# Kernel tuning notes

Hardware: AMD Instinct MI355X
Metric: run time of the kernel (lower is better)

The kernel has to match this reference:

```python
import jax, jax.numpy as jnp
import numpy as np

EPS = 1e-5


def _layernorm(x, w, b):
    mu = jnp.mean(x, axis=-1, keepdims=True)
    xc = x - mu
    var = jnp.mean(xc * xc, axis=-1, keepdims=True)
    return xc * jax.lax.rsqrt(var + EPS) * w + b


def _s5_ssm(u, lam_re, lam_im, log_step, B_re, B_im, C_re, C_im, Dvec):
    # u: [B,L,D]; diagonal complex SSM with ZOH discretization + associative scan
    Lam = lam_re + 1j * lam_im                      # [P]
    step = jnp.exp(log_step)                        # [P]
    Abar = jnp.exp(Lam * step)                      # [P]
    Bbar = ((Abar - 1.0) / Lam)[:, None] * (B_re + 1j * B_im)  # [P,D]
    Bu = jnp.einsum('bld,pd->blp', u.astype(jnp.complex64), Bbar)  # [B,L,P]
    A_el = jnp.broadcast_to(Abar, Bu.shape)

    def binop(e1, e2):
        a1, b1 = e1
        a2, b2 = e2
        return a1 * a2, a2 * b1 + b2

    _, xs = jax.lax.associative_scan(binop, (A_el, Bu), axis=1)  # [B,L,P] complex
    y = jnp.einsum('blp,dp->bld', xs, C_re + 1j * C_im).real + Dvec * u
    return y


def _s5_block(x, an_w, an_b, lam_re, lam_im, log_step, B_re, B_im, C_re, C_im,
              Dvec, fn_w, fn_b, Wenc, Wdec):
    fx = _layernorm(x, an_w, an_b)
    s = _s5_ssm(fx, lam_re, lam_im, log_step, B_re, B_im, C_re, C_im, Dvec)
    z = jax.nn.gelu(s, approximate=False) + fx
    fy = _layernorm(z, fn_w, fn_b)
    h = fy @ Wenc.T                                  # [B,L,2D]
    a, g = jnp.split(h, 2, axis=-1)                  # GEGLU
    return (a * jax.nn.gelu(g, approximate=False)) @ Wdec.T + fy


def setup_inputs() -> dict:
    D = 1048   # d_model
    P = 1048   # state_dim
    NL = 3
    Bsz, L = 4, 4096
    key = jax.random.key(0)
    ks = jax.random.split(key, 20)
    f32 = jnp.float32
    inp = {}
    inp['x'] = jax.random.normal(ks[0], (Bsz, L, 1), f32)
    inp['enc_w'] = jax.random.normal(ks[1], (D, 1), f32)
    inp['enc_b'] = jnp.zeros((D,), f32)
    inp['norm_w'] = jnp.ones((NL, D), f32)
    inp['norm_b'] = jnp.zeros((NL, D), f32)
    inp['attn_norm_w'] = jnp.ones((NL, D), f32)
    inp['attn_norm_b'] = jnp.zeros((NL, D), f32)
    inp['ff_norm_w'] = jnp.ones((NL, D), f32)
    inp['ff_norm_b'] = jnp.zeros((NL, D), f32)
    # stable diagonal dynamics: Re(Lambda) < 0
    inp['lam_re'] = -0.5 * jax.random.uniform(ks[2], (NL, P), f32) - 0.05
    inp['lam_im'] = np.float32(np.pi) * jax.random.normal(ks[3], (NL, P), f32)
    lo, hi = np.float32(np.log(1e-3)), np.float32(np.log(1e-1))
    inp['log_step'] = lo + (hi - lo) * jax.random.uniform(ks[4], (NL, P), f32)
    sB = np.float32(1.0 / np.sqrt(D))
    sC = np.float32(1.0 / np.sqrt(P))
    inp['B_re'] = sB * jax.random.normal(ks[5], (NL, P, D), f32)
    inp['B_im'] = sB * jax.random.normal(ks[6], (NL, P, D), f32)
    inp['C_re'] = sC * jax.random.normal(ks[7], (NL, D, P), f32)
    inp['C_im'] = sC * jax.random.normal(ks[8], (NL, D, P), f32)
    inp['Dvec'] = jax.random.normal(ks[9], (NL, D), f32)
    sW = np.float32(1.0 / np.sqrt(D))
    inp['Wenc'] = sW * jax.random.normal(ks[10], (NL, 2 * D, D), f32)
    inp['Wdec'] = sW * jax.random.normal(ks[11], (NL, D, D), f32)
    inp['head_w'] = sW * jax.random.normal(ks[12], (1, D), f32)
    inp['head_b'] = jnp.zeros((1,), f32)
    return inp


def reference(x, enc_w, enc_b, norm_w, norm_b, attn_norm_w, attn_norm_b,
              ff_norm_w, ff_norm_b, lam_re, lam_im, log_step, B_re, B_im,
              C_re, C_im, Dvec, Wenc, Wdec, head_w, head_b):
    h = x @ enc_w.T + enc_b                          # [B,L,D]
    n_layers = norm_w.shape[0]
    for i in range(n_layers):                        # small fixed loop over layers
        z = _layernorm(h, norm_w[i], norm_b[i])      # prenorm
        z = _s5_block(z, attn_norm_w[i], attn_norm_b[i], lam_re[i], lam_im[i],
                      log_step[i], B_re[i], B_im[i], C_re[i], C_im[i],
                      Dvec[i], ff_norm_w[i], ff_norm_b[i], Wenc[i], Wdec[i])
        h = h + z                                    # residual (dropout = identity in eval)
    pooled = jnp.mean(h, axis=1)                     # [B,D]
    y = (pooled @ head_w.T + head_b).squeeze(-1)     # [B]
    return y
```

## Files before the change

### kernel.cpp

```cpp
#include <hip/hip_runtime.h>
#include <hip/hip_bf16.h>
#include <cstddef>

typedef __hip_bfloat16 bf16;

#define D_MODEL 1048
#define P_DIM   1048
#define NLAYER  3
#define BSZ     4
#define LSEQ    4096
#define BL      (BSZ*LSEQ)
#define BLD     ((size_t)BL*D_MODEL)
#define KP      1056
#define NP      1152
#define BLA     ((size_t)BL*KP)
#define NPKP    ((size_t)NP*KP)

#define NC      64
#define CL      (LSEQ/NC)
#define NSCAN   (BSZ*NC*P_DIM)
#define P2      (P_DIM/2)
#define NSCAN2  (BSZ*NC*P2)

typedef __attribute__((ext_vector_type(8))) short short8;
typedef __attribute__((ext_vector_type(4))) float f32x4;

#define TM 128
#define TN 128
#define TK 32
#define TILE_SH (TM*TK)
#define NGEMM   ((BL/TM)*(NP/TN))
#define KSTEPS  (KP/TK)

__device__ __forceinline__ float gelu_f(float x) {
    return 0.5f * x * (1.f + erff(x * 0.70710678118654752f));
}

__device__ __forceinline__ void tile_coords(int id, int& m0, int& n0) {
    int xcd  = id & 7;
    int slot = id >> 3;
    int xg   = slot / 9;
    int j    = slot - xg*9;
    m0 = (xg*8 + xcd) * TM;
    n0 = j * TN;
}

__device__ __forceinline__ void stage_tile(
    const bf16* __restrict__ src, int row0, int k0, short* lds, int tid)
{
#pragma unroll
    for (int c = 0; c < 2; ++c) {
        int chunk = tid + 256*c;
        int r = chunk >> 2;
        int col = ((chunk ^ (r >> 1)) & 3) * 8;
        __builtin_amdgcn_global_load_lds(
            (const __attribute__((address_space(1))) void*)(src + (size_t)(row0 + r)*KP + k0 + col),
            (__attribute__((address_space(3))) void*)(lds + chunk*8), 16, 0, 0);
    }
}

__device__ __forceinline__ void stage512(
    const bf16* __restrict__ src, int row0, int k0, short* lds, int tid)
{
    int r = tid >> 2;
    int col = ((tid ^ (r >> 1)) & 3) * 8;
    __builtin_amdgcn_global_load_lds(
        (const __attribute__((address_space(1))) void*)(src + (size_t)(row0 + r)*KP + k0 + col),
        (__attribute__((address_space(3))) void*)(lds + tid*8), 16, 0, 0);
}

__device__ __forceinline__ void mfma_step1(
    const short* As, const short* Ws, f32x4 (&acc)[4][4],
    int wm, int wn, int row_in, int qs)
{
    short8 a[4], b[4];
#pragma unroll
    for (int i = 0; i < 4; ++i) {
        a[i] = *(const short8*)&As[(wm + i*16 + row_in)*TK + qs];
        b[i] = *(const short8*)&Ws[(wn + i*16 + row_in)*TK + qs];
    }
#pragma unroll
    for (int i = 0; i < 4; ++i)
#pragma unroll
        for (int j = 0; j < 4; ++j)
            acc[i][j] = __builtin_amdgcn_mfma_f32_16x16x32_bf16(a[i], b[j], acc[i][j], 0, 0, 0);
}

#define ROT3(p0, p1, p2) { short* _t = p0; p0 = p1; p1 = p2; p2 = _t; }

template <int MODE>
__global__ __launch_bounds__(512, 4) void gemm2o_k(
    const bf16* __restrict__ A, const bf16* __restrict__ W0,
    const bf16* __restrict__ W1,
    bf16* __restrict__ O0, bf16* __restrict__ O1, int N)
{
    __shared__ __align__(16) short smem[9*TILE_SH];
    short *pA  = smem,             *pA1  = smem + TILE_SH,   *pA2  = smem + 2*TILE_SH;
    short *pW0 = smem + 3*TILE_SH, *pW01 = smem + 4*TILE_SH, *pW02 = smem + 5*TILE_SH;
    short *pW1 = smem + 6*TILE_SH, *pW11 = smem + 7*TILE_SH, *pW12 = smem + 8*TILE_SH;
    const int tid  = threadIdx.x;
    int m0, n0;
    tile_coords(blockIdx.x, m0, n0);
    const int wave = tid >> 6, lane = tid & 63;
    const int wr = wave >> 2, wc = wave & 3;
    const int wm = wr * 64;
    const int wn = (wc & 1) * 64;
    const bool useW1 = (wc >= 2);
    const int row_in = lane & 15;
    const int qs = (((lane >> 4) ^ (lane >> 1)) & 3) * 8;

    f32x4 acc[4][4] = {};

    stage512(A,  m0, 0,    pA,   tid);
    stage512(W0, n0, 0,    pW0,  tid);
    stage512(W1, n0, 0,    pW1,  tid);
    stage512(A,  m0, TK,   pA1,  tid);
    stage512(W0, n0, TK,   pW01, tid);
    stage512(W1, n0, TK,   pW11, tid);
    stage512(A,  m0, 2*TK, pA2,  tid);
    stage512(W0, n0, 2*TK, pW02, tid);
    stage512(W1, n0, 2*TK, pW12, tid);

    for (int s = 0; s <= KSTEPS - 4; ++s) {
        asm volatile("s_waitcnt vmcnt(6)" ::: "memory");
        __builtin_amdgcn_s_barrier();
        mfma_step1(pA, useW1 ? pW1 : pW0, acc, wm, wn, row_in, qs);
        __builtin_amdgcn_s_barrier();
        const int k0 = (s + 3) * TK;
        stage512(A,  m0, k0, pA,  tid);
        stage512(W0, n0, k0, pW0, tid);
        stage512(W1, n0, k0, pW1, tid);
        ROT3(pA,  pA1,  pA2);
        ROT3(pW0, pW01, pW02);
        ROT3(pW1, pW11, pW12);
    }
    asm volatile("s_waitcnt vmcnt(6)" ::: "memory");
    __builtin_amdgcn_s_barrier();
    mfma_step1(pA, useW1 ? pW1 : pW0, acc, wm, wn, row_in, qs);
    asm volatile("s_waitcnt vmcnt(3)" ::: "memory");
    __builtin_amdgcn_s_barrier();
    mfma_step1(pA1, useW1 ? pW11 : pW01, acc, wm, wn, row_in, qs);
    asm volatile("s_waitcnt vmcnt(0)" ::: "memory");
    __builtin_amdgcn_s_barrier();
    mfma_step1(pA2, useW1 ? pW12 : pW02, acc, wm, wn, row_in, qs);

    const int quad = lane >> 4;
    if (MODE == 0) {
        bf16* O = useW1 ? O1 : O0;
#pragma unroll
        for (int i = 0; i < 4; ++i) {
#pragma unroll
            for (int j = 0; j < 4; ++j) {
                int n = n0 + wn + j*16 + row_in;
#pragma unroll
                for (int r = 0; r < 4; ++r) {
                    int m = m0 + wm + i*16 + quad*4 + r;
                    size_t o = (size_t)m*KP + n;
                    if (n < N)        O[o] = __float2bfloat16(acc[i][j][r]);
                    else if (n < KP)  O[o] = __float2bfloat16(0.f);
                }
            }
        }
    } else {
        f32x4* xb = (f32x4*)smem;
        const int pp = wr*2 + (wc & 1);
#pragma unroll
        for (int ih = 0; ih < 2; ++ih) {
            __syncthreads();
            if (useW1) {
#pragma unroll
                for (int il = 0; il < 2; ++il)
#pragma unroll
                    for (int j = 0; j < 4; ++j)
                        xb[(((pp*2 + il)*4 + j) << 6) + lane] = acc[2*ih + il][j];
            }
            __syncthreads();
            if (!useW1) {
#pragma unroll
                for (int il = 0; il < 2; ++il) {
                    int i = 2*ih + il;
#pragma unroll
                    for (int j = 0; j < 4; ++j) {
                        f32x4 g = xb[(((pp*2 + il)*4 + j) << 6) + lane];
                        int n = n0 + wn + j*16 + row_in;
#pragma unroll
                        for (int r = 0; r < 4; ++r) {
                            int m = m0 + wm + i*16 + quad*4 + r;
                            size_t o = (size_t)m*KP + n;
                            if (n < N)        O0[o] = __float2bfloat16(acc[i][j][r] * gelu_f(g[r]));
                            else if (n < KP)  O0[o] = __float2bfloat16(0.f);
                        }
                    }
                }
            }
        }
    }
}

__global__ __launch_bounds__(256, 2) void gemmC_k(
    const bf16* __restrict__ A0, const bf16* __restrict__ W0,
    const bf16* __restrict__ A1, const bf16* __restrict__ W1,
    const bf16* __restrict__ fx, const float* __restrict__ dv,
    bf16* __restrict__ O, int N)
{
    __shared__ __align__(16) short As[2][TILE_SH];
    __shared__ __align__(16) short Ws[2][TILE_SH];
    const int tid  = threadIdx.x;
    int m0, n0;
    tile_coords(blockIdx.x, m0, n0);
    const int wave = tid >> 6, lane = tid & 63;
    const int wm = (wave >> 1) * 64, wn = (wave & 1) * 64;
    const int row_in = lane & 15;
    const int qs = (((lane >> 4) ^ (lane >> 1)) & 3) * 8;

    f32x4 acc[4][4] = {};

    const int NST = 2*KSTEPS;
    stage_tile(A0, m0, 0,  As[0], tid);
    stage_tile(W0, n0, 0,  Ws[0], tid);
    stage_tile(A0, m0, TK, As[1], tid);
    stage_tile(W0, n0, TK, Ws[1], tid);

    for (int s = 0; s < NST - 1; ++s) {
        asm volatile("s_waitcnt vmcnt(4)" ::: "memory");
        __builtin_amdgcn_s_barrier();
        mfma_step1(As[s & 1], Ws[s & 1], acc, wm, wn, row_in, qs);
        __builtin_amdgcn_s_barrier();
        if (s < NST - 2) {
            int t = s + 2;
            const bf16* A = (t >= KSTEPS) ? A1 : A0;
            const bf16* W = (t >= KSTEPS) ? W1 : W0;
            int kk = (t >= KSTEPS) ? t - KSTEPS : t;
            stage_tile(A, m0, kk*TK, As[s & 1], tid);
            stage_tile(W, n0, kk*TK, Ws[s & 1], tid);
        }
    }
    asm volatile("s_waitcnt vmcnt(0)" ::: "memory");
    __builtin_amdgcn_s_barrier();
    mfma_step1(As[(NST-1) & 1], Ws[(NST-1) & 1], acc, wm, wn, row_in, qs);

    const int quad = lane >> 4;
#pragma unroll
    for (int i = 0; i < 4; ++i) {
#pragma unroll
        for (int j = 0; j < 4; ++j) {
            int n = n0 + wn + j*16 + row_in;
#pragma unroll
            for (int r = 0; r < 4; ++r) {
                int m = m0 + wm + i*16 + quad*4 + r;
                size_t o = (size_t)m*KP + n;
                if (n < N) {
                    float f = __bfloat162float(fx[o]);
                    float t = acc[i][j][r] + dv[n]*f;
                    O[o] = __float2bfloat16(gelu_f(t) + f);
                } else if (n < KP) {
                    O[o] = __float2bfloat16(0.f);
                }
            }
        }
    }
}

__global__ __launch_bounds__(256, 2) void gemmD_k(
    const bf16* __restrict__ A, const bf16* __restrict__ W,
    const bf16* __restrict__ fy, float* __restrict__ h, int N)
{
    __shared__ __align__(16) short As[2][TILE_SH];
    __shared__ __align__(16) short Ws[2][TILE_SH];
    const int tid  = threadIdx.x;
    int m0, n0;
    tile_coords(blockIdx.x, m0, n0);
    const int wave = tid >> 6, lane = tid & 63;
    const int wm = (wave >> 1) * 64, wn = (wave & 1) * 64;
    const int row_in = lane & 15;
    const int qs = (((lane >> 4) ^ (lane >> 1)) & 3) * 8;

    f32x4 acc[4][4] = {};

    stage_tile(A, m0, 0,  As[0], tid);
    stage_tile(W, n0, 0,  Ws[0], tid);
    stage_tile(A, m0, TK, As[1], tid);
    stage_tile(W, n0, TK, Ws[1], tid);

    for (int s = 0; s < KSTEPS - 1; ++s) {
        asm volatile("s_waitcnt vmcnt(4)" ::: "memory");
        __builtin_amdgcn_s_barrier();
        mfma_step1(As[s & 1], Ws[s & 1], acc, wm, wn, row_in, qs);
        __builtin_amdgcn_s_barrier();
        if (s < KSTEPS - 2) {
            const int k0 = (s + 2) * TK;
            stage_tile(A, m0, k0, As[s & 1], tid);
            stage_tile(W, n0, k0, Ws[s & 1], tid);
        }
    }
    asm volatile("s_waitcnt vmcnt(0)" ::: "memory");
    __builtin_amdgcn_s_barrier();
    mfma_step1(As[(KSTEPS-1) & 1], Ws[(KSTEPS-1) & 1], acc, wm, wn, row_in, qs);

    const int quad = lane >> 4;
#pragma unroll
    for (int i = 0; i < 4; ++i) {
#pragma unroll
        for (int j = 0; j < 4; ++j) {
            int n = n0 + wn + j*16 + row_in;
            if (n >= N) continue;
#pragma unroll
            for (int r = 0; r < 4; ++r) {
                int m = m0 + wm + i*16 + quad*4 + r;
                float f = __bfloat162float(fy[(size_t)m*KP + n]);
                h[(size_t)m*D_MODEL + n] += acc[i][j][r] + f;
            }
        }
    }
}

__global__ __launch_bounds__(256) void prepconv_k(
    const float* __restrict__ lam_re, const float* __restrict__ lam_im,
    const float* __restrict__ log_step,
    const float* __restrict__ B_re, const float* __restrict__ B_im,
    bf16* __restrict__ bbar_re, bf16* __restrict__ bbar_im,
    float* __restrict__ abar,
    const float* __restrict__ s0, const float* __restrict__ s1,
    const float* __restrict__ s2, const float* __restrict__ s3,
    const float* __restrict__ s4, bf16* __restrict__ w5)
{
    size_t idx = (size_t)blockIdx.x*256 + threadIdx.x;
    if (idx >= NPKP) return;
    int z = blockIdx.z;
    int p = (int)(idx / KP);
    int d = (int)(idx - (size_t)p*KP);
    if (z == 0) {
        if (p >= P_DIM || d >= D_MODEL) {
            bbar_re[idx] = __float2bfloat16(0.f);
            bbar_im[idx] = __float2bfloat16(0.f);
            return;
        }
        float lr = lam_re[p], li = lam_im[p];
        float st = expf(log_step[p]);
        float er = expf(lr*st);
        float ar = er * cosf(li*st);
        float ai = er * sinf(li*st);
        if (d == 0) { abar[p] = ar; abar[P_DIM + p] = ai; }
        float den = lr*lr + li*li;
        float xr = ar - 1.f, xi = ai;
        float cr = (xr*lr + xi*li) / den;
        float ci = (xi*lr - xr*li) / den;
        float br = B_re[(size_t)p*D_MODEL + d], bi = B_im[(size_t)p*D_MODEL + d];
        bbar_re[idx] = __float2bfloat16(cr*br - ci*bi);
        bbar_im[idx] = __float2bfloat16(cr*bi + ci*br);
    } else {
        int w = z - 1;
        const float* src = (w == 0) ? s0 : (w == 1) ? s1 : (w == 2) ? s2 : (w == 3) ? s3 : s4;
        float scale = (w == 1) ? -1.f : 1.f;
        float v = (p < D_MODEL && d < D_MODEL) ? scale*src[(size_t)p*D_MODEL + d] : 0.f;
        w5[(size_t)w*NPKP + idx] = __float2bfloat16(v);
    }
}

__device__ __forceinline__ float2 block_reduce2(float a, float b) {
    __syncthreads();
    for (int off = 32; off; off >>= 1) {
        a += __shfl_down(a, off, 64);
        b += __shfl_down(b, off, 64);
    }
    __shared__ float sa[4], sb[4];
    int lane = threadIdx.x & 63, wv = threadIdx.x >> 6;
    if (lane == 0) { sa[wv] = a; sb[wv] = b; }
    __syncthreads();
    if (threadIdx.x == 0) {
        sa[0] = sa[0]+sa[1]+sa[2]+sa[3];
        sb[0] = sb[0]+sb[1]+sb[2]+sb[3];
    }
    __syncthreads();
    return make_float2(sa[0], sb[0]);
}

template <int ENC>
__global__ __launch_bounds__(256) void ln2x_k(
    const float* __restrict__ xin,
    const float* __restrict__ ew, const float* __restrict__ eb,
    float* __restrict__ hbuf,
    const float* __restrict__ w1, const float* __restrict__ bb1,
    const float* __restrict__ w2, const float* __restrict__ bb2,
    bf16* __restrict__ y)
{
    const size_t row = blockIdx.x;
    float v[5];
    float s = 0.f, ss = 0.f;
    int i = 0;
    if (ENC) {
        float xv = xin[row];
        float* hr = hbuf + row * D_MODEL;
        for (int d = threadIdx.x; d < KP; d += 256, ++i) {
            float t = 0.f;
            if (d < D_MODEL) { t = xv*ew[d] + eb[d]; hr[d] = t; }
            v[i] = t; s += t; ss += t*t;
        }
    } else {
        const float* xr = hbuf + row * D_MODEL;
        for (int d = threadIdx.x; d < KP; d += 256, ++i) {
            float t = (d < D_MODEL) ? xr[d] : 0.f;
            v[i] = t; s += t; ss += t*t;
        }
    }
    float2 r = block_reduce2(s, ss);
    float mu  = r.x * (1.f/D_MODEL);
    float var = r.y * (1.f/D_MODEL) - mu*mu;
    float inv = rsqrtf(var + 1e-5f);
    s = 0.f; ss = 0.f; i = 0;
    for (int d = threadIdx.x; d < KP; d += 256, ++i) {
        float z = (d < D_MODEL) ? (v[i]-mu)*inv*w1[d] + bb1[d] : 0.f;
        v[i] = z; s += z; ss += z*z;
    }
    r = block_reduce2(s, ss);
    mu  = r.x * (1.f/D_MODEL);
    var = r.y * (1.f/D_MODEL) - mu*mu;
    inv = rsqrtf(var + 1e-5f);
    bf16* yr = y + row * KP;
    i = 0;
    for (int d = threadIdx.x; d < KP; d += 256, ++i) {
        float o = (d < D_MODEL) ? (v[i]-mu)*inv*w2[d] + bb2[d] : 0.f;
        yr[d] = __float2bfloat16(o);
    }
}

__global__ __launch_bounds__(256) void ln_k(
    const bf16* __restrict__ x, const float* __restrict__ w,
    const float* __restrict__ b, bf16* __restrict__ y)
{
    const size_t row = blockIdx.x;
    const bf16* xr = x + row * KP;
    float v[5];
    float s = 0.f, ss = 0.f;
    int i = 0;
    for (int d = threadIdx.x; d < KP; d += 256, ++i) {
        float t = (d < D_MODEL) ? __bfloat162float(xr[d]) : 0.f;
        v[i] = t; s += t; ss += t*t;
    }
    float2 r = block_reduce2(s, ss);
    float mu  = r.x * (1.f/D_MODEL);
    float var = r.y * (1.f/D_MODEL) - mu*mu;
    float inv = rsqrtf(var + 1e-5f);
    bf16* yr = y + row * KP;
    i = 0;
    for (int d = threadIdx.x; d < KP; d += 256, ++i) {
        float o = (d < D_MODEL) ? (v[i]-mu)*inv*w[d] + b[d] : 0.f;
        yr[d] = __float2bfloat16(o);
    }
}

__device__ __forceinline__ float2 bf2f(unsigned int u) {
    unsigned int lo = u << 16, hi = u & 0xffff0000u;
    float2 r;
    r.x = __uint_as_float(lo);
    r.y = __uint_as_float(hi);
    return r;
}
__device__ __forceinline__ unsigned int f2bf2(float a, float b) {
    bf16 ba = __float2bfloat16(a), bb = __float2bfloat16(b);
    unsigned short ua = *(unsigned short*)&ba, ub = *(unsigned short*)&bb;
    return (unsigned int)ua | ((unsigned int)ub << 16);
}

__global__ __launch_bounds__(256) void scan_partial_k(
    const unsigned int* __restrict__ ur, const unsigned int* __restrict__ ui,
    const float* __restrict__ abar,
    float* __restrict__ sum_re, float* __restrict__ sum_im)
{
    int idx = blockIdx.x*256 + threadIdx.x;
    if (idx >= NSCAN2) return;
    int p2 = idx % P2;
    int rest = idx / P2;
    int c = rest % NC, b = rest / NC;
    int p = 2*p2;
    float ar0 = abar[p],   ai0 = abar[P_DIM + p];
    float ar1 = abar[p+1], ai1 = abar[P_DIM + p + 1];
    size_t base = (((size_t)b*LSEQ + (size_t)c*CL)*KP + p) >> 1;
    float s0r = 0.f, s0i = 0.f, s1r = 0.f, s1i = 0.f;
    for (int i = 0; i < CL; ++i) {
        size_t o = base + (size_t)i*(KP/2);
        float2 br = bf2f(ur[o]);
        float2 bi = bf2f(ui[o]);
        float n0r = fmaf(ar0, s0r, fmaf(-ai0, s0i, br.x));
        float n0i = fmaf(ar0, s0i, fmaf( ai0, s0r, bi.x));
        float n1r = fmaf(ar1, s1r, fmaf(-ai1, s1i, br.y));
        float n1i = fmaf(ar1, s1i, fmaf( ai1, s1r, bi.y));
        s0r = n0r; s0i = n0i; s1r = n1r; s1i = n1i;
    }
    size_t so = ((size_t)b*NC + c)*P_DIM + p;
    *(float2*)&sum_re[so] = make_float2(s0r, s1r);
    *(float2*)&sum_im[so] = make_float2(s0i, s1i);
}

__global__ __launch_bounds__(256) void scan_carry_k(
    const float* __restrict__ sum_re, const float* __restrict__ sum_im,
    const float* __restrict__ abar,
    float* __restrict__ car_re, float* __restrict__ car_im)
{
    int idx = blockIdx.x*256 + threadIdx.x;
    if (idx >= BSZ*P_DIM) return;
    int p = idx % P_DIM, b = idx / P_DIM;
    float cr = abar[p], ci = abar[P_DIM + p];
#pragma unroll
    for (int s = 0; s < 6; ++s) {
        float nr = cr*cr - ci*ci;
        float ni = 2.f*cr*ci;
        cr = nr; ci = ni;
    }
    float xre = 0.f, xim = 0.f;
    size_t base = (size_t)b*NC*P_DIM + p;
    for (int c = 0; c < NC; ++c) {
        size_t o = base + (size_t)c*P_DIM;
        car_re[o] = xre; car_im[o] = xim;
        float sre = sum_re[o], sim = sum_im[o];
        float nr = fmaf(cr, xre, fmaf(-ci, xim, sre));
        float ni = fmaf(cr, xim, fmaf( ci, xre, sim));
        xre = nr; xim = ni;
    }
}

__global__ __launch_bounds__(256) void scan_apply_k(
    unsigned int* __restrict__ ur, unsigned int* __restrict__ ui,
    const float* __restrict__ abar,
    const float* __restrict__ car_re, const float* __restrict__ car_im)
{
    int idx = blockIdx.x*256 + threadIdx.x;
    if (idx >= NSCAN2) return;
    int p2 = idx % P2;
    int rest = idx / P2;
    int c = rest % NC, b = rest / NC;
    int p = 2*p2;
    float ar0 = abar[p],   ai0 = abar[P_DIM + p];
    float ar1 = abar[p+1], ai1 = abar[P_DIM + p + 1];
    size_t co = ((size_t)b*NC + c)*P_DIM + p;
    float2 c_r = *(const float2*)&car_re[co];
    float2 c_i = *(const float2*)&car_im[co];
    float x0r = c_r.x, x0i = c_i.x, x1r = c_r.y, x1i = c_i.y;
    size_t base = (((size_t)b*LSEQ + (size_t)c*CL)*KP + p) >> 1;
    for (int i = 0; i < CL; ++i) {
        size_t o = base + (size_t)i*(KP/2);
        float2 br = bf2f(ur[o]);
        float2 bi = bf2f(ui[o]);
        float n0r = fmaf(ar0, x0r, fmaf(-ai0, x0i, br.x));
        float n0i = fmaf(ar0, x0i, fmaf( ai0, x0r, bi.x));
        float n1r = fmaf(ar1, x1r, fmaf(-ai1, x1i, br.y));
        float n1i = fmaf(ar1, x1i, fmaf( ai1, x1r, bi.y));
        x0r = n0r; x0i = n0i; x1r = n1r; x1i = n1i;
        ur[o] = f2bf2(x0r, x1r);
        ui[o] = f2bf2(x0i, x1i);
    }
}

__global__ void head_init_k(float* out, const float* hb)
{
    if (threadIdx.x < BSZ) out[threadIdx.x] = hb[0];
}

__global__ __launch_bounds__(256) void head_k(
    const float* __restrict__ h, const float* __restrict__ hw,
    float* __restrict__ out)
{
    int b = blockIdx.x;
    int chunk = blockIdx.y;
    const float* hb = h + ((size_t)b*LSEQ + (size_t)chunk*64)*D_MODEL;
    float s = 0.f;
    for (int l = 0; l < 64; ++l) {
        const float* hr = hb + (size_t)l*D_MODEL;
        for (int d = threadIdx.x; d < D_MODEL; d += 256)
            s += hr[d]*hw[d];
    }
    for (int off = 32; off; off >>= 1) s += __shfl_down(s, off, 64);
    __shared__ float sm[4];
    int lane = threadIdx.x & 63, wv = threadIdx.x >> 6;
    if (lane == 0) sm[wv] = s;
    __syncthreads();
    if (threadIdx.x == 0)
        atomicAdd(out + b, (sm[0]+sm[1]+sm[2]+sm[3]) * (1.f/LSEQ));
}

extern "C" void kernel_launch(void* const* d_in, const int* in_sizes, int n_in,
                              void* d_out, int out_size, void* d_ws, size_t ws_size,
                              hipStream_t stream)
{
    const float* x          = (const float*)d_in[0];
    const float* enc_w      = (const float*)d_in[1];
    const float* enc_b      = (const float*)d_in[2];
    const float* norm_w     = (const float*)d_in[3];
    const float* norm_b     = (const float*)d_in[4];
    const float* attn_w     = (const float*)d_in[5];
    const float* attn_b     = (const float*)d_in[6];
    const float* ff_w       = (const float*)d_in[7];
    const float* ff_b       = (const float*)d_in[8];
    const float* lam_re     = (const float*)d_in[9];
    const float* lam_im     = (const float*)d_in[10];
    const float* log_step   = (const float*)d_in[11];
    const float* B_re       = (const float*)d_in[12];
    const float* B_im       = (const float*)d_in[13];
    const float* C_re       = (const float*)d_in[14];
    const float* C_im       = (const float*)d_in[15];
    const float* Dvec       = (const float*)d_in[16];
    const float* Wenc       = (const float*)d_in[17];
    const float* Wdec       = (const float*)d_in[18];
    const float* head_w     = (const float*)d_in[19];
    const float* head_b     = (const float*)d_in[20];
    float* out = (float*)d_out;

    float* h    = (float*)d_ws;
    bf16*  b1   = (bf16*)(h + BLD);
    bf16*  b2   = b1 + BLA;
    bf16*  b3   = b2 + BLA;
    bf16*  b4   = b3 + BLA;
    bf16*  wbr  = b4 + BLA;
    bf16*  wbi  = wbr + NPKP;
    bf16*  w5   = wbi + NPKP;
    bf16*  wcr  = w5;
    bf16*  wci  = w5 + NPKP;
    bf16*  wea  = w5 + 2*NPKP;
    bf16*  weg  = w5 + 3*NPKP;
    bf16*  wd   = w5 + 4*NPKP;
    float* abar = (float*)(w5 + 5*NPKP);
    float* sum_re = abar + 2*P_DIM;
    float* sum_im = sum_re + NSCAN;
    float* car_re = sum_im + NSCAN;
    float* car_im = car_re + NSCAN;

    const int CV   = (int)((NPKP + 255)/256);
    const int SC_G = (NSCAN2 + 255)/256;
    const size_t pd = (size_t)P_DIM*D_MODEL;

    for (int i = 0; i < NLAYER; ++i) {
        const float* WencA = Wenc + (size_t)i*2*pd;
        const float* WencG = WencA + pd;
        prepconv_k<<<dim3(CV,1,6), 256, 0, stream>>>(
            lam_re + i*P_DIM, lam_im + i*P_DIM, log_step + i*P_DIM,
            B_re + i*pd, B_im + i*pd, wbr, wbi, abar,
            C_re + i*pd, C_im + i*pd, WencA, WencG, Wdec + i*pd, w5);

        if (i == 0)
            ln2x_k<1><<<BL, 256, 0, stream>>>(x, enc_w, enc_b, h,
                norm_w + i*D_MODEL, norm_b + i*D_MODEL,
                attn_w + i*D_MODEL, attn_b + i*D_MODEL, b2);
        else
            ln2x_k<0><<<BL, 256, 0, stream>>>(nullptr, nullptr, nullptr, h,
                norm_w + i*D_MODEL, norm_b + i*D_MODEL,
                attn_w + i*D_MODEL, attn_b + i*D_MODEL, b2);

        gemm2o_k<0><<<NGEMM, 512, 0, stream>>>(b2, wbr, wbi, b1, b3, P_DIM);

        scan_partial_k<<<SC_G, 256, 0, stream>>>((unsigned int*)b1, (unsigned int*)b3,
                                                 abar, sum_re, sum_im);
        scan_carry_k<<<(BSZ*P_DIM + 255)/256, 256, 0, stream>>>(sum_re, sum_im, abar, car_re, car_im);
        scan_apply_k<<<SC_G, 256, 0, stream>>>((unsigned int*)b1, (unsigned int*)b3,
                                               abar, car_re, car_im);

        gemmC_k<<<NGEMM, 256, 0, stream>>>(b1, wcr, b3, wci, b2, Dvec + i*D_MODEL, b4, D_MODEL);

        ln_k<<<BL, 256, 0, stream>>>(b4, ff_w + i*D_MODEL, ff_b + i*D_MODEL, b1);

        gemm2o_k<1><<<NGEMM, 512, 0, stream>>>(b1, wea, weg, b2, nullptr, D_MODEL);

        gemmD_k<<<NGEMM, 256, 0, stream>>>(b2, wd, b1, h, D_MODEL);
    }

    head_init_k<<<1, 64, 0, stream>>>(out, head_b);
    head_k<<<dim3(BSZ, 64), 256, 0, stream>>>(h, head_w, out);
}
```

Measured before the change: 1.916 ms.

## Enlarge GEMM tiles to 256x128 with 128x64 per-wave subtiles and MFMA priority

Doubles the M tile of all three GEMM kernels to 256 rows, so each wave now computes a 128x64 subtile with 8x4 MFMA accumulators. This reuses each staged W fragment across more A rows and cuts global and LDS traffic per FLOP. The dual-output kernel drops its triple-buffered pipeline for double buffering, and s_setprio is raised around the MFMA blocks. In exchange, per-thread register pressure roughly doubles and occupancy falls (launch bounds go from 4 to 2 blocks for gemm2o). Halving the tile count also risks poorer CU load balance.

```diff
diff --git a/kernel.cpp b/kernel.cpp
--- a/kernel.cpp
+++ b/kernel.cpp
@@ -25,12 +25,15 @@
 typedef __attribute__((ext_vector_type(8))) short short8;
 typedef __attribute__((ext_vector_type(4))) float f32x4;
 
-#define TM 128
+#define TM 256
 #define TN 128
 #define TK 32
-#define TILE_SH (TM*TK)
-#define NGEMM   ((BL/TM)*(NP/TN))
+#define ASH2 (TM*TK)
+#define WSH  (TN*TK)
+#define SLOTC (ASH2 + WSH)
+#define SLOT2 (ASH2 + 2*WSH)
 #define KSTEPS  (KP/TK)
+#define NGEMM ((BL/TM)*(NP/TN))
 
 __device__ __forceinline__ float gelu_f(float x) {
     return 0.5f * x * (1.f + erff(x * 0.70710678118654752f));
@@ -45,21 +48,46 @@
     n0 = j * TN;
 }
 
-__device__ __forceinline__ void stage_tile(
+__device__ __forceinline__ void stageA_t256(
     const bf16* __restrict__ src, int row0, int k0, short* lds, int tid)
 {
 #pragma unroll
-    for (int c = 0; c < 2; ++c) {
-        int chunk = tid + 256*c;
-        int r = chunk >> 2;
-        int col = ((chunk ^ (r >> 1)) & 3) * 8;
+    for (int c0 = 0; c0 < 4; ++c0) {
+        int c = tid + 256*c0;
+        int r = c >> 2;
+        int col = ((c ^ (r >> 1)) & 3) * 8;
         __builtin_amdgcn_global_load_lds(
             (const __attribute__((address_space(1))) void*)(src + (size_t)(row0 + r)*KP + k0 + col),
-            (__attribute__((address_space(3))) void*)(lds + chunk*8), 16, 0, 0);
-    }
-}
-
-__device__ __forceinline__ void stage512(
+            (__attribute__((address_space(3))) void*)(lds + c*8), 16, 0, 0);
+    }
+}
+__device__ __forceinline__ void stageW_t256(
+    const bf16* __restrict__ src, int row0, int k0, short* lds, int tid)
+{
+#pragma unroll
+    for (int c0 = 0; c0 < 2; ++c0) {
+        int c = tid + 256*c0;
+        int r = c >> 2;
+        int col = ((c ^ (r >> 1)) & 3) * 8;
+        __builtin_amdgcn_global_load_lds(
+            (const __attribute__((address_space(1))) void*)(src + (size_t)(row0 + r)*KP + k0 + col),
+            (__attribute__((address_space(3))) void*)(lds + c*8), 16, 0, 0);
+    }
+}
+__device__ __forceinline__ void stageA_t512(
+    const bf16* __restrict__ src, int row0, int k0, short* lds, int tid)
+{
+#pragma unroll
+    for (int c0 = 0; c0 < 2; ++c0) {
+        int c = tid + 512*c0;
+        int r = c >> 2;
+        int col = ((c ^ (r >> 1)) & 3) * 8;
+        __builtin_amdgcn_global_load_lds(
+            (const __attribute__((address_space(1))) void*)(src + (size_t)(row0 + r)*KP + k0 + col),
+            (__attribute__((address_space(3))) void*)(lds + c*8), 16, 0, 0);
+    }
+}
+__device__ __forceinline__ void stageW_t512(
     const bf16* __restrict__ src, int row0, int k0, short* lds, int tid)
 {
     int r = tid >> 2;
@@ -69,86 +97,74 @@
         (__attribute__((address_space(3))) void*)(lds + tid*8), 16, 0, 0);
 }
 
-__device__ __forceinline__ void mfma_step1(
-    const short* As, const short* Ws, f32x4 (&acc)[4][4],
+__device__ __forceinline__ void mfma_big(
+    const short* As, const short* Ws, f32x4 (&acc)[8][4],
     int wm, int wn, int row_in, int qs)
 {
-    short8 a[4], b[4];
-#pragma unroll
-    for (int i = 0; i < 4; ++i) {
+    short8 a[8], b[4];
+#pragma unroll
+    for (int i = 0; i < 8; ++i)
         a[i] = *(const short8*)&As[(wm + i*16 + row_in)*TK + qs];
-        b[i] = *(const short8*)&Ws[(wn + i*16 + row_in)*TK + qs];
-    }
-#pragma unroll
-    for (int i = 0; i < 4; ++i)
+#pragma unroll
+    for (int j = 0; j < 4; ++j)
+        b[j] = *(const short8*)&Ws[(wn + j*16 + row_in)*TK + qs];
+#pragma unroll
+    for (int i = 0; i < 8; ++i)
 #pragma unroll
         for (int j = 0; j < 4; ++j)
             acc[i][j] = __builtin_amdgcn_mfma_f32_16x16x32_bf16(a[i], b[j], acc[i][j], 0, 0, 0);
 }
 
-#define ROT3(p0, p1, p2) { short* _t = p0; p0 = p1; p1 = p2; p2 = _t; }
-
 template <int MODE>
-__global__ __launch_bounds__(512, 4) void gemm2o_k(
+__global__ __launch_bounds__(512, 2) void gemm2o_k(
     const bf16* __restrict__ A, const bf16* __restrict__ W0,
     const bf16* __restrict__ W1,
     bf16* __restrict__ O0, bf16* __restrict__ O1, int N)
 {
-    __shared__ __align__(16) short smem[9*TILE_SH];
-    short *pA  = smem,             *pA1  = smem + TILE_SH,   *pA2  = smem + 2*TILE_SH;
-    short *pW0 = smem + 3*TILE_SH, *pW01 = smem + 4*TILE_SH, *pW02 = smem + 5*TILE_SH;
-    short *pW1 = smem + 6*TILE_SH, *pW11 = smem + 7*TILE_SH, *pW12 = smem + 8*TILE_SH;
+    __shared__ __align__(16) short smem[2*SLOT2];
     const int tid  = threadIdx.x;
     int m0, n0;
     tile_coords(blockIdx.x, m0, n0);
     const int wave = tid >> 6, lane = tid & 63;
-    const int wr = wave >> 2, wc = wave & 3;
-    const int wm = wr * 64;
-    const int wn = (wc & 1) * 64;
-    const bool useW1 = (wc >= 2);
+    const int g = wave >> 2;
+    const int u = wave & 3;
+    const int wm = (u >> 1) * 128, wn = (u & 1) * 64;
     const int row_in = lane & 15;
     const int qs = (((lane >> 4) ^ (lane >> 1)) & 3) * 8;
 
-    f32x4 acc[4][4] = {};
-
-    stage512(A,  m0, 0,    pA,   tid);
-    stage512(W0, n0, 0,    pW0,  tid);
-    stage512(W1, n0, 0,    pW1,  tid);
-    stage512(A,  m0, TK,   pA1,  tid);
-    stage512(W0, n0, TK,   pW01, tid);
-    stage512(W1, n0, TK,   pW11, tid);
-    stage512(A,  m0, 2*TK, pA2,  tid);
-    stage512(W0, n0, 2*TK, pW02, tid);
-    stage512(W1, n0, 2*TK, pW12, tid);
-
-    for (int s = 0; s <= KSTEPS - 4; ++s) {
-        asm volatile("s_waitcnt vmcnt(6)" ::: "memory");
+    f32x4 acc[8][4] = {};
+
+#define STG2(s) { int _s=(s); short* _b = smem + (_s&1)*SLOT2; \
+    stageA_t512(A,  m0, _s*TK, _b, tid); \
+    stageW_t512(W0, n0, _s*TK, _b + ASH2, tid); \
+    stageW_t512(W1, n0, _s*TK, _b + ASH2 + WSH, tid); }
+
+    STG2(0); STG2(1);
+    for (int s = 0; s < KSTEPS - 1; ++s) {
+        asm volatile("s_waitcnt vmcnt(4)" ::: "memory");
         __builtin_amdgcn_s_barrier();
-        mfma_step1(pA, useW1 ? pW1 : pW0, acc, wm, wn, row_in, qs);
+        short* base = smem + (s & 1)*SLOT2;
+        __builtin_amdgcn_s_setprio(1);
+        mfma_big(base, base + ASH2 + g*WSH, acc, wm, wn, row_in, qs);
+        __builtin_amdgcn_s_setprio(0);
         __builtin_amdgcn_s_barrier();
-        const int k0 = (s + 3) * TK;
-        stage512(A,  m0, k0, pA,  tid);
-        stage512(W0, n0, k0, pW0, tid);
-        stage512(W1, n0, k0, pW1, tid);
-        ROT3(pA,  pA1,  pA2);
-        ROT3(pW0, pW01, pW02);
-        ROT3(pW1, pW11, pW12);
-    }
-    asm volatile("s_waitcnt vmcnt(6)" ::: "memory");
-    __builtin_amdgcn_s_barrier();
-    mfma_step1(pA, useW1 ? pW1 : pW0, acc, wm, wn, row_in, qs);
-    asm volatile("s_waitcnt vmcnt(3)" ::: "memory");
-    __builtin_amdgcn_s_barrier();
-    mfma_step1(pA1, useW1 ? pW11 : pW01, acc, wm, wn, row_in, qs);
+        if (s < KSTEPS - 2) STG2(s + 2);
+    }
     asm volatile("s_waitcnt vmcnt(0)" ::: "memory");
     __builtin_amdgcn_s_barrier();
-    mfma_step1(pA2, useW1 ? pW12 : pW02, acc, wm, wn, row_in, qs);
+    {
+        short* base = smem + ((KSTEPS-1) & 1)*SLOT2;
+        __builtin_amdgcn_s_setprio(1);
+        mfma_big(base, base + ASH2 + g*WSH, acc, wm, wn, row_in, qs);
+        __builtin_amdgcn_s_setprio(0);
+    }
+#undef STG2
 
     const int quad = lane >> 4;
     if (MODE == 0) {
-        bf16* O = useW1 ? O1 : O0;
-#pragma unroll
-        for (int i = 0; i < 4; ++i) {
+        bf16* O = g ? O1 : O0;
+#pragma unroll
+        for (int i = 0; i < 8; ++i) {
 #pragma unroll
             for (int j = 0; j < 4; ++j) {
                 int n = n0 + wn + j*16 + row_in;
@@ -163,31 +179,30 @@
         }
     } else {
         f32x4* xb = (f32x4*)smem;
-        const int pp = wr*2 + (wc & 1);
-#pragma unroll
-        for (int ih = 0; ih < 2; ++ih) {
+#pragma unroll
+        for (int ih = 0; ih < 4; ++ih) {
             __syncthreads();
-            if (useW1) {
+            if (g) {
 #pragma unroll
                 for (int il = 0; il < 2; ++il)
 #pragma unroll
                     for (int j = 0; j < 4; ++j)
-                        xb[(((pp*2 + il)*4 + j) << 6) + lane] = acc[2*ih + il][j];
+                        xb[(((u*2 + il)*4 + j) << 6) + lane] = acc[2*ih + il][j];
             }
             __syncthreads();
-            if (!useW1) {
+            if (!g) {
 #pragma unroll
                 for (int il = 0; il < 2; ++il) {
                     int i = 2*ih + il;
 #pragma unroll
                     for (int j = 0; j < 4; ++j) {
-                        f32x4 g = xb[(((pp*2 + il)*4 + j) << 6) + lane];
+                        f32x4 gv = xb[(((u*2 + il)*4 + j) << 6) + lane];
                         int n = n0 + wn + j*16 + row_in;
 #pragma unroll
                         for (int r = 0; r < 4; ++r) {
                             int m = m0 + wm + i*16 + quad*4 + r;
                             size_t o = (size_t)m*KP + n;
-                            if (n < N)        O0[o] = __float2bfloat16(acc[i][j][r] * gelu_f(g[r]));
+                            if (n < N)        O0[o] = __float2bfloat16(acc[i][j][r] * gelu_f(gv[r]));
                             else if (n < KP)  O0[o] = __float2bfloat16(0.f);
                         }
                     }
@@ -203,45 +218,50 @@
     const bf16* __restrict__ fx, const float* __restrict__ dv,
     bf16* __restrict__ O, int N)
 {
-    __shared__ __align__(16) short As[2][TILE_SH];
-    __shared__ __align__(16) short Ws[2][TILE_SH];
+    __shared__ __align__(16) short smem[2*SLOTC];
     const int tid  = threadIdx.x;
     int m0, n0;
     tile_coords(blockIdx.x, m0, n0);
     const int wave = tid >> 6, lane = tid & 63;
-    const int wm = (wave >> 1) * 64, wn = (wave & 1) * 64;
+    const int wm = (wave >> 1) * 128, wn = (wave & 1) * 64;
     const int row_in = lane & 15;
     const int qs = (((lane >> 4) ^ (lane >> 1)) & 3) * 8;
 
-    f32x4 acc[4][4] = {};
+    f32x4 acc[8][4] = {};
 
     const int NST = 2*KSTEPS;
-    stage_tile(A0, m0, 0,  As[0], tid);
-    stage_tile(W0, n0, 0,  Ws[0], tid);
-    stage_tile(A0, m0, TK, As[1], tid);
-    stage_tile(W0, n0, TK, Ws[1], tid);
-
+#define STGC(s) { int _s=(s); \
+    const bf16* _A = (_s >= KSTEPS) ? A1 : A0; \
+    const bf16* _W = (_s >= KSTEPS) ? W1 : W0; \
+    int _kk = (_s >= KSTEPS ? _s - KSTEPS : _s)*TK; \
+    short* _b = smem + (_s&1)*SLOTC; \
+    stageA_t256(_A, m0, _kk, _b, tid); \
+    stageW_t256(_W, n0, _kk, _b + ASH2, tid); }
+
+    STGC(0); STGC(1);
     for (int s = 0; s < NST - 1; ++s) {
-        asm volatile("s_waitcnt vmcnt(4)" ::: "memory");
+        asm volatile("s_waitcnt vmcnt(6)" ::: "memory");
         __builtin_amdgcn_s_barrier();
-        mfma_step1(As[s & 1], Ws[s & 1], acc, wm, wn, row_in, qs);
+        short* base = smem + (s & 1)*SLOTC;
+        __builtin_amdgcn_s_setprio(1);
+        mfma_big(base, base + ASH2, acc, wm, wn, row_in, qs);
+        __builtin_amdgcn_s_setprio(0);
         __builtin_amdgcn_s_barrier();
-        if (s < NST - 2) {
-            int t = s + 2;
-            const bf16* A = (t >= KSTEPS) ? A1 : A0;
-            const bf16* W = (t >= KSTEPS) ? W1 : W0;
-            int kk = (t >= KSTEPS) ? t - KSTEPS : t;
-            stage_tile(A, m0, kk*TK, As[s & 1], tid);
-            stage_tile(W, n0, kk*TK, Ws[s & 1], tid);
-        }
+        if (s < NST - 2) STGC(s + 2);
     }
     asm volatile("s_waitcnt vmcnt(0)" ::: "memory");
     __builtin_amdgcn_s_barrier();
-    mfma_step1(As[(NST-1) & 1], Ws[(NST-1) & 1], acc, wm, wn, row_in, qs);
+    {
+        short* base = smem + ((NST-1) & 1)*SLOTC;
+        __builtin_amdgcn_s_setprio(1);
+        mfma_big(base, base + ASH2, acc, wm, wn, row_in, qs);
+        __builtin_amdgcn_s_setprio(0);
+    }
+#undef STGC
 
     const int quad = lane >> 4;
 #pragma unroll
-    for (int i = 0; i < 4; ++i) {
+    for (int i = 0; i < 8; ++i) {
 #pragma unroll
         for (int j = 0; j < 4; ++j) {
             int n = n0 + wn + j*16 + row_in;
@@ -265,41 +285,45 @@
     const bf16* __restrict__ A, const bf16* __restrict__ W,
     const bf16* __restrict__ fy, float* __restrict__ h, int N)
 {
-    __shared__ __align__(16) short As[2][TILE_SH];
-    __shared__ __align__(16) short Ws[2][TILE_SH];
+    __shared__ __align__(16) short smem[2*SLOTC];
     const int tid  = threadIdx.x;
     int m0, n0;
     tile_coords(blockIdx.x, m0, n0);
     const int wave = tid >> 6, lane = tid & 63;
-    const int wm = (wave >> 1) * 64, wn = (wave & 1) * 64;
+    const int wm = (wave >> 1) * 128, wn = (wave & 1) * 64;
     const int row_in = lane & 15;
     const int qs = (((lane >> 4) ^ (lane >> 1)) & 3) * 8;
 
-    f32x4 acc[4][4] = {};
-
-    stage_tile(A, m0, 0,  As[0], tid);
-    stage_tile(W, n0, 0,  Ws[0], tid);
-    stage_tile(A, m0, TK, As[1], tid);
-    stage_tile(W, n0, TK, Ws[1], tid);
-
+    f32x4 acc[8][4] = {};
+
+#define STGD(s) { int _s=(s); short* _b = smem + (_s&1)*SLOTC; \
+    stageA_t256(A, m0, _s*TK, _b, tid); \
+    stageW_t256(W, n0, _s*TK, _b + ASH2, tid); }
+
+    STGD(0); STGD(1);
     for (int s = 0; s < KSTEPS - 1; ++s) {
-        asm volatile("s_waitcnt vmcnt(4)" ::: "memory");
+        asm volatile("s_waitcnt vmcnt(6)" ::: "memory");
         __builtin_amdgcn_s_barrier();
-        mfma_step1(As[s & 1], Ws[s & 1], acc, wm, wn, row_in, qs);
+        short* base = smem + (s & 1)*SLOTC;
+        __builtin_amdgcn_s_setprio(1);
+        mfma_big(base, base + ASH2, acc, wm, wn, row_in, qs);
+        __builtin_amdgcn_s_setprio(0);
         __builtin_amdgcn_s_barrier();
-        if (s < KSTEPS - 2) {
-            const int k0 = (s + 2) * TK;
-            stage_tile(A, m0, k0, As[s & 1], tid);
-            stage_tile(W, n0, k0, Ws[s & 1], tid);
-        }
+        if (s < KSTEPS - 2) STGD(s + 2);
     }
     asm volatile("s_waitcnt vmcnt(0)" ::: "memory");
     __builtin_amdgcn_s_barrier();
-    mfma_step1(As[(KSTEPS-1) & 1], Ws[(KSTEPS-1) & 1], acc, wm, wn, row_in, qs);
+    {
+        short* base = smem + ((KSTEPS-1) & 1)*SLOTC;
+        __builtin_amdgcn_s_setprio(1);
+        mfma_big(base, base + ASH2, acc, wm, wn, row_in, qs);
+        __builtin_amdgcn_s_setprio(0);
+    }
+#undef STGD
 
     const int quad = lane >> 4;
 #pragma unroll
-    for (int i = 0; i < 4; ++i) {
+    for (int i = 0; i < 8; ++i) {
 #pragma unroll
         for (int j = 0; j < 4; ++j) {
             int n = n0 + wn + j*16 + row_in;
```

Result: slower. 2.227 ms (+16.2%).
